# Kernel optimization log

Hardware: AMD Instinct MI355X
Metric: run time of the kernel (lower is better)

Reference implementation:

```python
import jax, jax.numpy as jnp
import numpy as np

NUM_HEADS = 8
NUM_POINTS = 4


def _bilinear(img, xs, ys):
    """Bilinear sample with zero padding (grid_sample align_corners=False).
    img: [N, H, W, C]; xs, ys: [N, P] pixel-space coords. Returns [N, P, C]."""
    H, W = img.shape[1], img.shape[2]
    x0 = jnp.floor(xs)
    y0 = jnp.floor(ys)
    wx = xs - x0
    wy = ys - y0
    x0i = x0.astype(jnp.int32)
    y0i = y0.astype(jnp.int32)

    def g(ix, iy):
        valid = ((ix >= 0) & (ix < W) & (iy >= 0) & (iy < H)).astype(img.dtype)
        ixc = jnp.clip(ix, 0, W - 1)
        iyc = jnp.clip(iy, 0, H - 1)
        v = jax.vmap(lambda im, yy, xx: im[yy, xx])(img, iyc, ixc)  # [N,P,C]
        return v * valid[..., None]

    return (g(x0i, y0i) * ((1 - wx) * (1 - wy))[..., None]
            + g(x0i + 1, y0i) * (wx * (1 - wy))[..., None]
            + g(x0i, y0i + 1) * ((1 - wx) * wy)[..., None]
            + g(x0i + 1, y0i + 1) * (wx * wy)[..., None])


def setup_inputs() -> dict:
    key = jax.random.key(0)
    ks = jax.random.split(key, 10)
    BN, C, H, W = 12, 256, 40, 100
    nq = H * W
    hp = NUM_HEADS * NUM_POINTS
    s = 1.0 / np.sqrt(C).astype(np.float32)
    return {
        "img_feats": jax.random.normal(ks[0], (BN, C, H, W), jnp.float32),
        "warp_grid": jax.random.uniform(ks[1], (BN, H, W, 2), jnp.float32),
        "reference_points": jax.random.uniform(ks[2], (BN, nq, 1, 2), jnp.float32),
        "Wv": jax.random.normal(ks[3], (C, C), jnp.float32) * s,
        "bv": jnp.zeros((C,), jnp.float32),
        "Woff": jax.random.normal(ks[4], (C, hp * 2), jnp.float32) * 0.01,
        "boff": jax.random.normal(ks[5], (hp * 2,), jnp.float32) * 0.5,
        "Wattn": jax.random.normal(ks[6], (C, hp), jnp.float32) * 0.01,
        "battn": jnp.zeros((hp,), jnp.float32),
        "Wout": jax.random.normal(ks[7], (C, C), jnp.float32) * s,
        "bout": jnp.zeros((C,), jnp.float32),
    }


def reference(img_feats, warp_grid, reference_points,
              Wv, bv, Woff, boff, Wattn, battn, Wout, bout):
    BN, C, H, W = img_feats.shape
    heads, pts = NUM_HEADS, NUM_POINTS
    hd = C // heads
    nq = H * W

    feat = img_feats.transpose(0, 2, 3, 1)  # [BN, H, W, C]

    # BEVWarp: bilinear warp of image features at the projected grid ([0,1] normed)
    gx = warp_grid[..., 0].reshape(BN, -1) * W - 0.5
    gy = warp_grid[..., 1].reshape(BN, -1) * H - 0.5
    warped = _bilinear(feat, gx, gy)          # [BN, nq, C] -> value
    query = feat.reshape(BN, nq, C)           # flattened img feats -> query

    # MultiScaleDeformableAttention, num_levels=1
    v = (warped @ Wv + bv).reshape(BN, nq, heads, hd)
    off = (query @ Woff + boff).reshape(BN, nq, heads, pts, 2)
    attn = jax.nn.softmax((query @ Wattn + battn).reshape(BN, nq, heads, pts), axis=-1)

    norm = jnp.array([W, H], dtype=img_feats.dtype)
    loc = reference_points.reshape(BN, nq, 1, 1, 2) + off / norm  # [BN,nq,h,p,2]

    vh = v.transpose(0, 2, 1, 3).reshape(BN * heads, H, W, hd)
    lx = (loc[..., 0] * W - 0.5).transpose(0, 2, 1, 3).reshape(BN * heads, nq * pts)
    ly = (loc[..., 1] * H - 0.5).transpose(0, 2, 1, 3).reshape(BN * heads, nq * pts)
    sampled = _bilinear(vh, lx, ly).reshape(BN, heads, nq, pts, hd)

    agg = jnp.einsum('bhqpd,bqhp->bqhd', sampled, attn).reshape(BN, nq, C)
    out = agg @ Wout + bout + query  # output_proj + residual (dropout=0 at eval)
    return out.transpose(0, 2, 1).reshape(BN, C, H, W)
```

## Files before the change

### kernel.cpp

```cpp
#include <hip/hip_runtime.h>

#define DEVINL __device__ __forceinline__

typedef __attribute__((ext_vector_type(4))) float f32x4;
typedef __attribute__((ext_vector_type(8))) short short8;

constexpr int kBN = 12, kC = 256, kH = 40, kW = 100;
constexpr int kNQ = kH * kW;
constexpr int kM = kBN * kNQ;

DEVINL float bflo(uint p) { union { uint i; float f; } v; v.i = p << 16; return v.f; }
DEVINL float bfhi(uint p) { union { uint i; float f; } v; v.i = p & 0xffff0000u; return v.f; }
DEVINL ushort f2bf(float f) {
  union { float f; uint i; } v; v.f = f;
  uint i = v.i;
  return (ushort)((i + 0x7fffu + ((i >> 16) & 1u)) >> 16);
}
DEVINL uint pack2(float a, float b) { return (uint)f2bf(a) | ((uint)f2bf(b) << 16); }

DEVINL void mfma_bf16(f32x4& acc, short8 a, short8 b) {
  acc = __builtin_amdgcn_mfma_f32_16x16x32_bf16(a, b, acc, 0, 0, 0);
}

DEVINL void gload16(const ushort* g, char* lds) {
  __builtin_amdgcn_global_load_lds(
      (const __attribute__((address_space(1))) uint*)g,
      (__attribute__((address_space(3))) uint*)lds, 16, 0, 0);
}

DEVINL void acc8(float* acc, uint4 d, float wv) {
  acc[0] += wv * bflo(d.x); acc[1] += wv * bfhi(d.x);
  acc[2] += wv * bflo(d.y); acc[3] += wv * bfhi(d.y);
  acc[4] += wv * bflo(d.z); acc[5] += wv * bfhi(d.z);
  acc[6] += wv * bflo(d.w); acc[7] += wv * bfhi(d.w);
}

__global__ __launch_bounds__(256) void k_wt(const float* __restrict__ W,
                                            ushort* __restrict__ WT, int K, int N) {
  int idx = blockIdx.x * 256 + threadIdx.x;
  if (idx >= K * N) return;
  int n = idx / K, k = idx - n * K;
  WT[idx] = f2bf(W[k * N + n]);
}

__global__ __launch_bounds__(256) void k_transpose(const float* __restrict__ img,
                                                   ushort* __restrict__ feat) {
  __shared__ ushort tile[64][66];
  int b = blockIdx.z, c0 = blockIdx.y * 64, q0 = blockIdx.x * 64;
  int t = threadIdx.x;
  int ql = t & 63, cl = t >> 6;
#pragma unroll
  for (int i = 0; i < 16; ++i) {
    int c = cl + i * 4, q = q0 + ql;
    float v = (q < kNQ) ? img[(size_t)(b * kC + c0 + c) * kNQ + q] : 0.f;
    tile[c][ql] = f2bf(v);
  }
  __syncthreads();
  int cc = t & 63, qr = t >> 6;
#pragma unroll
  for (int i = 0; i < 16; ++i) {
    int qlo = qr + i * 4, q = q0 + qlo;
    if (q < kNQ) feat[(size_t)(b * kNQ + q) * kC + c0 + cc] = tile[cc][qlo];
  }
}

__global__ __launch_bounds__(256) void k_warp(const ushort* __restrict__ feat,
                                              const float* __restrict__ grid,
                                              ushort* __restrict__ warped) {
  int orig = blockIdx.x;
  int n = (orig & 7) * 750 + (orig >> 3);
  int t = threadIdx.x;
  int ql = t >> 5, g = t & 31;
  int gq = n * 8 + ql;
  int b = gq / kNQ;
  float gx = grid[(size_t)gq * 2 + 0] * kW - 0.5f;
  float gy = grid[(size_t)gq * 2 + 1] * kH - 0.5f;
  float x0f = floorf(gx), y0f = floorf(gy);
  int x0 = (int)x0f, y0 = (int)y0f;
  float wx = gx - x0f, wy = gy - y0f;
  float acc[8];
#pragma unroll
  for (int i = 0; i < 8; ++i) acc[i] = 0.f;
  const ushort* fb = feat + (size_t)b * kNQ * kC + g * 8;
#pragma unroll
  for (int ty = 0; ty < 2; ++ty) {
    int iy = y0 + ty;
    if (iy < 0 || iy >= kH) continue;
    float wyv = ty ? wy : 1.f - wy;
#pragma unroll
    for (int tx = 0; tx < 2; ++tx) {
      int ix = x0 + tx;
      if (ix < 0 || ix >= kW) continue;
      float wv = wyv * (tx ? wx : 1.f - wx);
      uint4 d = *(const uint4*)(fb + (size_t)(iy * kW + ix) * kC);
      acc8(acc, d, wv);
    }
  }
  uint o[4] = {pack2(acc[0], acc[1]), pack2(acc[2], acc[3]),
               pack2(acc[4], acc[5]), pack2(acc[6], acc[7])};
  *(uint4*)(warped + (size_t)gq * kC + g * 8) = *(uint4*)o;
}

template <int EPI>
__global__ __launch_bounds__(256) void k_gemm256(const ushort* __restrict__ A,
                                                 const ushort* __restrict__ BT,
                                                 const float* __restrict__ bias,
                                                 ushort* __restrict__ Obf,
                                                 float* __restrict__ Ofp,
                                                 const float* __restrict__ resid) {
  extern __shared__ char smem[];
  char* As = smem;
  char* Bs = smem + 4096;
  const int t = threadIdx.x, wave = t >> 6, lane = t & 63;
  const int l15 = lane & 15, l4 = lane >> 4;
  const int b = blockIdx.x / 63, mb = blockIdx.x % 63;
  const int q0 = mb * 64;
  const int nrows = (kNQ - q0 < 64) ? (kNQ - q0) : 64;
  const int n0w = wave * 64;
  const int ra = t >> 2, ca = t & 3;
  const int sca = ca ^ ((ra >> 1) & 3);
  const ushort* gA = A + ((size_t)b * kNQ + q0 + ra) * 256 + sca * 8;
  const ushort* gB = BT + (size_t)ra * 256 + sca * 8;
  const bool doA = (ra < nrows);

  f32x4 acc[4][4];
#pragma unroll
  for (int i = 0; i < 4; ++i)
#pragma unroll
    for (int j = 0; j < 4; ++j) acc[i][j] = (f32x4)0.f;

  for (int kk = 0; kk < 256; kk += 32) {
    if (doA) gload16(gA + kk, As + t * 16);
#pragma unroll
    for (int i = 0; i < 4; ++i)
      gload16(gB + (size_t)i * 64 * 256 + kk, Bs + (i * 256 + t) * 16);
    __syncthreads();
    short8 af[4], bf[4];
#pragma unroll
    for (int mf = 0; mf < 4; ++mf) {
      int r = mf * 16 + l15;
      int sl = l4 ^ ((r >> 1) & 3);
      af[mf] = *(const short8*)(As + r * 64 + sl * 16);
    }
#pragma unroll
    for (int nf = 0; nf < 4; ++nf) {
      int r = n0w + nf * 16 + l15;
      int sl = l4 ^ ((r >> 1) & 3);
      bf[nf] = *(const short8*)(Bs + r * 64 + sl * 16);
    }
#pragma unroll
    for (int mf = 0; mf < 4; ++mf)
#pragma unroll
      for (int nf = 0; nf < 4; ++nf) mfma_bf16(acc[mf][nf], af[mf], bf[nf]);
    __syncthreads();
  }

  if (EPI == 0) {
#pragma unroll
    for (int mf = 0; mf < 4; ++mf) {
      if (mf * 16 >= nrows) continue;
      int q = q0 + mf * 16 + l4 * 4;
#pragma unroll
      for (int nf = 0; nf < 4; ++nf) {
        int col = n0w + nf * 16 + l15;
        float bv = bias[col];
        int h = col >> 5, ch = col & 31;
        ushort* dst = Obf + (size_t)(b * 8 + h) * kNQ * 32 + ch;
#pragma unroll
        for (int j = 0; j < 4; ++j)
          dst[(size_t)(q + j) * 32] = f2bf(acc[mf][nf][j] + bv);
      }
    }
  } else {
    float* Tw = (float*)(smem + wave * 4352);
#pragma unroll
    for (int nf = 0; nf < 4; ++nf) {
      float bv = bias[n0w + nf * 16 + l15];
#pragma unroll
      for (int mf = 0; mf < 4; ++mf)
#pragma unroll
        for (int j = 0; j < 4; ++j)
          Tw[l15 * 68 + mf * 16 + l4 * 4 + j] = acc[mf][nf][j] + bv;
      int c = l15, hi = l4;
      int rs = hi * 16;
      if (rs < nrows) {
        int col = n0w + nf * 16 + c;
        size_t gi = ((size_t)b * kC + col) * kNQ + q0 + rs;
#pragma unroll
        for (int k = 0; k < 4; ++k) {
          float4 tv = *(float4*)(&Tw[c * 68 + rs + k * 4]);
          float4 rv = *(const float4*)(resid + gi + k * 4);
          tv.x += rv.x; tv.y += rv.y; tv.z += rv.z; tv.w += rv.w;
          *(float4*)(Ofp + gi + k * 4) = tv;
        }
      }
    }
  }
}

__global__ __launch_bounds__(256) void k_offattn(const ushort* __restrict__ A,
                                                 const ushort* __restrict__ WoffT,
                                                 const ushort* __restrict__ WattnT,
                                                 const float* __restrict__ boff,
                                                 const float* __restrict__ battn,
                                                 const float* __restrict__ refp,
                                                 float4* __restrict__ samp) {
  extern __shared__ char smem[];
  char* As = smem;
  char* Bs = smem + 4096;
  float* T = (float*)smem;
  const int t = threadIdx.x, wave = t >> 6, lane = t & 63;
  const int l15 = lane & 15, l4 = lane >> 4;
  const int b = blockIdx.x / 63, mb = blockIdx.x % 63;
  const int q0 = mb * 64;
  const int nrows = (kNQ - q0 < 64) ? (kNQ - q0) : 64;
  const int wr = wave >> 1, wc = wave & 1;
  const int ra = t >> 2, ca = t & 3;
  const int sca = ca ^ ((ra >> 1) & 3);
  const ushort* gA = A + ((size_t)b * kNQ + q0 + ra) * 256 + sca * 8;
  const ushort* gB0 = WoffT + (size_t)ra * 256 + sca * 8;
  const ushort* gB1 = WattnT + (size_t)ra * 256 + sca * 8;
  const bool doA = (ra < nrows);

  f32x4 acc[2][3];
#pragma unroll
  for (int i = 0; i < 2; ++i)
#pragma unroll
    for (int j = 0; j < 3; ++j) acc[i][j] = (f32x4)0.f;

  for (int kk = 0; kk < 256; kk += 32) {
    if (doA) gload16(gA + kk, As + t * 16);
    gload16(gB0 + kk, Bs + t * 16);
    if (t < 128) gload16(gB1 + kk, Bs + (256 + t) * 16);
    __syncthreads();
    short8 af[2], bf[3];
#pragma unroll
    for (int mf = 0; mf < 2; ++mf) {
      int r = wr * 32 + mf * 16 + l15;
      int sl = l4 ^ ((r >> 1) & 3);
      af[mf] = *(const short8*)(As + r * 64 + sl * 16);
    }
#pragma unroll
    for (int nf = 0; nf < 3; ++nf) {
      int r = wc * 48 + nf * 16 + l15;
      int sl = l4 ^ ((r >> 1) & 3);
      bf[nf] = *(const short8*)(Bs + r * 64 + sl * 16);
    }
#pragma unroll
    for (int mf = 0; mf < 2; ++mf)
#pragma unroll
      for (int nf = 0; nf < 3; ++nf) mfma_bf16(acc[mf][nf], af[mf], bf[nf]);
    __syncthreads();
  }

#pragma unroll
  for (int nf = 0; nf < 3; ++nf) {
    int col = wc * 48 + nf * 16 + l15;
    float bv = (col < 64) ? boff[col] : battn[col - 64];
#pragma unroll
    for (int mf = 0; mf < 2; ++mf)
#pragma unroll
      for (int j = 0; j < 4; ++j) {
        int row = wr * 32 + mf * 16 + l4 * 4 + j;
        T[row * 101 + col] = acc[mf][nf][j] + bv;
      }
  }
  __syncthreads();
  int row = t >> 2;
  if (row < nrows) {
    int q = q0 + row;
    float refx = refp[((size_t)b * kNQ + q) * 2 + 0] * kW - 0.5f;
    float refy = refp[((size_t)b * kNQ + q) * 2 + 1] * kH - 0.5f;
#pragma unroll
    for (int hi2 = 0; hi2 < 2; ++hi2) {
      int h = (t & 3) + hi2 * 4;
      float sx[4], sy[4], lg[4];
#pragma unroll
      for (int p = 0; p < 4; ++p) {
        sx[p] = refx + T[row * 101 + h * 8 + p * 2 + 0];
        sy[p] = refy + T[row * 101 + h * 8 + p * 2 + 1];
        lg[p] = T[row * 101 + 64 + h * 4 + p];
      }
      float mx = fmaxf(fmaxf(lg[0], lg[1]), fmaxf(lg[2], lg[3]));
      float e[4], s = 0.f;
#pragma unroll
      for (int p = 0; p < 4; ++p) { e[p] = __expf(lg[p] - mx); s += e[p]; }
      float inv = 1.f / s;
      float4* dst = samp + ((size_t)(b * 8 + h) * kNQ + q) * 4;
#pragma unroll
      for (int p = 0; p < 4; ++p) dst[p] = make_float4(sx[p], sy[p], e[p] * inv, 0.f);
    }
  }
}

__global__ __launch_bounds__(256) void k_sample(const ushort* __restrict__ v,
                                                const float4* __restrict__ samp,
                                                ushort* __restrict__ agg) {
  int orig = blockIdx.x;
  int n = (orig & 7) * 756 + (orig >> 3);
  int plane = n / 63, chunk = n - plane * 63;
  int t = threadIdx.x;
  int ql = t >> 2, g = t & 3;
  int q = chunk * 64 + ql;
  if (q >= kNQ) return;
  int b = plane >> 3, h = plane & 7;
  const ushort* pv = v + (size_t)plane * kNQ * 32 + g * 8;
  const int lane = t & 63, gbase = lane & ~3;

  float4 mys = samp[((size_t)plane * kNQ + q) * 4 + g];
  float acc[8];
#pragma unroll
  for (int i = 0; i < 8; ++i) acc[i] = 0.f;
#pragma unroll
  for (int p = 0; p < 4; ++p) {
    float sxp = __shfl(mys.x, gbase + p);
    float syp = __shfl(mys.y, gbase + p);
    float wp  = __shfl(mys.z, gbase + p);
    float x0f = floorf(sxp), y0f = floorf(syp);
    int x0 = (int)x0f, y0 = (int)y0f;
    float wx = sxp - x0f, wy = syp - y0f;
#pragma unroll
    for (int ty = 0; ty < 2; ++ty) {
      int iy = y0 + ty;
      if (iy < 0 || iy >= kH) continue;
      float wyv = ty ? wy : 1.f - wy;
#pragma unroll
      for (int tx = 0; tx < 2; ++tx) {
        int ix = x0 + tx;
        if (ix < 0 || ix >= kW) continue;
        float wv = wp * wyv * (tx ? wx : 1.f - wx);
        uint4 d = *(const uint4*)(pv + (size_t)(iy * kW + ix) * 32);
        acc8(acc, d, wv);
      }
    }
  }
  uint o[4] = {pack2(acc[0], acc[1]), pack2(acc[2], acc[3]),
               pack2(acc[4], acc[5]), pack2(acc[6], acc[7])};
  *(uint4*)(agg + ((size_t)b * kNQ + q) * kC + h * 32 + g * 8) = *(uint4*)o;
}

extern "C" void kernel_launch(void* const* d_in, const int* in_sizes, int n_in,
                              void* d_out, int out_size, void* d_ws, size_t ws_size,
                              hipStream_t stream) {
  const float* img   = (const float*)d_in[0];
  const float* grid  = (const float*)d_in[1];
  const float* refp  = (const float*)d_in[2];
  const float* Wv    = (const float*)d_in[3];
  const float* bv    = (const float*)d_in[4];
  const float* Woff  = (const float*)d_in[5];
  const float* boff  = (const float*)d_in[6];
  const float* Wattn = (const float*)d_in[7];
  const float* battn = (const float*)d_in[8];
  const float* Wout  = (const float*)d_in[9];
  const float* bout  = (const float*)d_in[10];
  float* out = (float*)d_out;

  char* ws = (char*)d_ws;
  const size_t SZ = (size_t)kM * kC * 2;
  ushort* feat   = (ushort*)(ws);
  ushort* warped = (ushort*)(ws + SZ);
  ushort* vbuf   = (ushort*)(ws + 2 * SZ);
  float4* samp   = (float4*)(ws + 3 * SZ);
  ushort* WvT    = (ushort*)(ws + 4 * SZ);
  ushort* WoffT  = (ushort*)(ws + 4 * SZ + 131072);
  ushort* WattnT = (ushort*)(ws + 4 * SZ + 131072 + 32768);
  ushort* WoutT  = (ushort*)(ws + 4 * SZ + 131072 + 32768 + 16384);
  ushort* aggb   = warped;

  k_wt<<<(65536 + 255) / 256, 256, 0, stream>>>(Wv, WvT, 256, 256);
  k_wt<<<(16384 + 255) / 256, 256, 0, stream>>>(Woff, WoffT, 256, 64);
  k_wt<<<(8192 + 255) / 256, 256, 0, stream>>>(Wattn, WattnT, 256, 32);
  k_wt<<<(65536 + 255) / 256, 256, 0, stream>>>(Wout, WoutT, 256, 256);

  k_transpose<<<dim3(63, 4, 12), 256, 0, stream>>>(img, feat);
  k_warp<<<6000, 256, 0, stream>>>(feat, grid, warped);
  k_gemm256<0><<<756, 256, 20480, stream>>>(warped, WvT, bv, vbuf, nullptr, nullptr);
  k_offattn<<<756, 256, 25856, stream>>>(feat, WoffT, WattnT, boff, battn, refp, samp);
  k_sample<<<6048, 256, 0, stream>>>(vbuf, samp, aggb);
  k_gemm256<1><<<756, 256, 20480, stream>>>(aggb, WoutT, bout, nullptr, out, img);
}
```

Measured before the change: 135.1 us.

## Fuse offset/attn GEMM, deformable sampling and output projection into one kernel

Merges the offset/attention projection, softmax, bilinear deformable sampling and output projection with residual into a single per-tile kernel. The sample parameters and aggregated values now stay in LDS instead of round-tripping through global memory. The four weight-transpose launches are also merged into one, and block indices are remapped across XCDs. In exchange the fused kernel needs about 58KB of LDS, which lowers occupancy, and the gather phase uses only 756 blocks with a serial loop over heads, so latency hiding during sampling may drop.

After: 162.1 us. 1.2x slower.

```diff
diff --git a/kernel.cpp b/kernel.cpp
--- a/kernel.cpp
+++ b/kernel.cpp
@@ -35,12 +35,24 @@
   acc[6] += wv * bflo(d.w); acc[7] += wv * bfhi(d.w);
 }
 
-__global__ __launch_bounds__(256) void k_wt(const float* __restrict__ W,
-                                            ushort* __restrict__ WT, int K, int N) {
+__global__ __launch_bounds__(256) void k_wt_all(const float* __restrict__ Wv,
+                                                const float* __restrict__ Woff,
+                                                const float* __restrict__ Wattn,
+                                                const float* __restrict__ Wout,
+                                                ushort* __restrict__ WvT,
+                                                ushort* __restrict__ WoffT,
+                                                ushort* __restrict__ WattnT,
+                                                ushort* __restrict__ WoutT) {
   int idx = blockIdx.x * 256 + threadIdx.x;
-  if (idx >= K * N) return;
-  int n = idx / K, k = idx - n * K;
-  WT[idx] = f2bf(W[k * N + n]);
+  const float* W; ushort* WT; int N, base;
+  if (idx < 65536)       { W = Wv;    WT = WvT;    N = 256; base = 0; }
+  else if (idx < 81920)  { W = Woff;  WT = WoffT;  N = 64;  base = 65536; }
+  else if (idx < 90112)  { W = Wattn; WT = WattnT; N = 32;  base = 81920; }
+  else if (idx < 155648) { W = Wout;  WT = WoutT;  N = 256; base = 90112; }
+  else return;
+  int i = idx - base;
+  int n = i >> 8, k = i & 255;
+  WT[i] = f2bf(W[k * N + n]);
 }
 
 __global__ __launch_bounds__(256) void k_transpose(const float* __restrict__ img,
@@ -101,13 +113,10 @@
   *(uint4*)(warped + (size_t)gq * kC + g * 8) = *(uint4*)o;
 }
 
-template <int EPI>
-__global__ __launch_bounds__(256) void k_gemm256(const ushort* __restrict__ A,
-                                                 const ushort* __restrict__ BT,
-                                                 const float* __restrict__ bias,
-                                                 ushort* __restrict__ Obf,
-                                                 float* __restrict__ Ofp,
-                                                 const float* __restrict__ resid) {
+__global__ __launch_bounds__(256) void k_gemmv(const ushort* __restrict__ A,
+                                               const ushort* __restrict__ BT,
+                                               const float* __restrict__ bias,
+                                               ushort* __restrict__ Obf) {
   extern __shared__ char smem[];
   char* As = smem;
   char* Bs = smem + 4096;
@@ -155,118 +164,107 @@
     __syncthreads();
   }
 
-  if (EPI == 0) {
-#pragma unroll
-    for (int mf = 0; mf < 4; ++mf) {
-      if (mf * 16 >= nrows) continue;
-      int q = q0 + mf * 16 + l4 * 4;
-#pragma unroll
-      for (int nf = 0; nf < 4; ++nf) {
-        int col = n0w + nf * 16 + l15;
-        float bv = bias[col];
-        int h = col >> 5, ch = col & 31;
-        ushort* dst = Obf + (size_t)(b * 8 + h) * kNQ * 32 + ch;
-#pragma unroll
-        for (int j = 0; j < 4; ++j)
-          dst[(size_t)(q + j) * 32] = f2bf(acc[mf][nf][j] + bv);
-      }
-    }
-  } else {
-    float* Tw = (float*)(smem + wave * 4352);
+#pragma unroll
+  for (int mf = 0; mf < 4; ++mf) {
+    if (mf * 16 >= nrows) continue;
+    int q = q0 + mf * 16 + l4 * 4;
 #pragma unroll
     for (int nf = 0; nf < 4; ++nf) {
-      float bv = bias[n0w + nf * 16 + l15];
-#pragma unroll
-      for (int mf = 0; mf < 4; ++mf)
-#pragma unroll
-        for (int j = 0; j < 4; ++j)
-          Tw[l15 * 68 + mf * 16 + l4 * 4 + j] = acc[mf][nf][j] + bv;
-      int c = l15, hi = l4;
-      int rs = hi * 16;
-      if (rs < nrows) {
-        int col = n0w + nf * 16 + c;
-        size_t gi = ((size_t)b * kC + col) * kNQ + q0 + rs;
-#pragma unroll
-        for (int k = 0; k < 4; ++k) {
-          float4 tv = *(float4*)(&Tw[c * 68 + rs + k * 4]);
-          float4 rv = *(const float4*)(resid + gi + k * 4);
-          tv.x += rv.x; tv.y += rv.y; tv.z += rv.z; tv.w += rv.w;
-          *(float4*)(Ofp + gi + k * 4) = tv;
-        }
-      }
-    }
-  }
-}
-
-__global__ __launch_bounds__(256) void k_offattn(const ushort* __restrict__ A,
-                                                 const ushort* __restrict__ WoffT,
-                                                 const ushort* __restrict__ WattnT,
-                                                 const float* __restrict__ boff,
-                                                 const float* __restrict__ battn,
-                                                 const float* __restrict__ refp,
-                                                 float4* __restrict__ samp) {
+      int col = n0w + nf * 16 + l15;
+      float bv = bias[col];
+      int h = col >> 5, ch = col & 31;
+      ushort* dst = Obf + (size_t)(b * 8 + h) * kNQ * 32 + ch;
+#pragma unroll
+      for (int j = 0; j < 4; ++j)
+        dst[(size_t)(q + j) * 32] = f2bf(acc[mf][nf][j] + bv);
+    }
+  }
+}
+
+__global__ __launch_bounds__(256) void k_mega(const ushort* __restrict__ feat,
+                                              const ushort* __restrict__ WoffT,
+                                              const ushort* __restrict__ WattnT,
+                                              const float* __restrict__ boff,
+                                              const float* __restrict__ battn,
+                                              const float* __restrict__ refp,
+                                              const ushort* __restrict__ vbuf,
+                                              const ushort* __restrict__ WoutT,
+                                              const float* __restrict__ bout,
+                                              const float* __restrict__ resid,
+                                              float* __restrict__ out) {
   extern __shared__ char smem[];
-  char* As = smem;
-  char* Bs = smem + 4096;
-  float* T = (float*)smem;
+  float* T  = (float*)smem;
+  char* As1 = smem + 26624;
+  char* Bs1 = smem + 26624 + 4096;
+  char* Ag  = smem + 26624;
+  char* Bs3 = smem;
+
   const int t = threadIdx.x, wave = t >> 6, lane = t & 63;
   const int l15 = lane & 15, l4 = lane >> 4;
-  const int b = blockIdx.x / 63, mb = blockIdx.x % 63;
+
+  int orig = blockIdx.x;
+  int xcd = orig % 8, ii = orig / 8;
+  int n = (xcd < 4 ? xcd * 95 : 380 + (xcd - 4) * 94) + ii;
+  const int b = n / 63, mb = n % 63;
   const int q0 = mb * 64;
   const int nrows = (kNQ - q0 < 64) ? (kNQ - q0) : 64;
+
   const int wr = wave >> 1, wc = wave & 1;
   const int ra = t >> 2, ca = t & 3;
   const int sca = ca ^ ((ra >> 1) & 3);
-  const ushort* gA = A + ((size_t)b * kNQ + q0 + ra) * 256 + sca * 8;
+  const ushort* gA  = feat + ((size_t)b * kNQ + q0 + ra) * 256 + sca * 8;
   const ushort* gB0 = WoffT + (size_t)ra * 256 + sca * 8;
   const ushort* gB1 = WattnT + (size_t)ra * 256 + sca * 8;
   const bool doA = (ra < nrows);
 
-  f32x4 acc[2][3];
-#pragma unroll
-  for (int i = 0; i < 2; ++i)
-#pragma unroll
-    for (int j = 0; j < 3; ++j) acc[i][j] = (f32x4)0.f;
-
-  for (int kk = 0; kk < 256; kk += 32) {
-    if (doA) gload16(gA + kk, As + t * 16);
-    gload16(gB0 + kk, Bs + t * 16);
-    if (t < 128) gload16(gB1 + kk, Bs + (256 + t) * 16);
-    __syncthreads();
-    short8 af[2], bf[3];
-#pragma unroll
-    for (int mf = 0; mf < 2; ++mf) {
-      int r = wr * 32 + mf * 16 + l15;
-      int sl = l4 ^ ((r >> 1) & 3);
-      af[mf] = *(const short8*)(As + r * 64 + sl * 16);
-    }
+  {
+    f32x4 acc1[2][3];
+#pragma unroll
+    for (int i = 0; i < 2; ++i)
+#pragma unroll
+      for (int j = 0; j < 3; ++j) acc1[i][j] = (f32x4)0.f;
+
+    for (int kk = 0; kk < 256; kk += 32) {
+      if (doA) gload16(gA + kk, As1 + t * 16);
+      gload16(gB0 + kk, Bs1 + t * 16);
+      if (t < 128) gload16(gB1 + kk, Bs1 + (256 + t) * 16);
+      __syncthreads();
+      short8 af[2], bf[3];
+#pragma unroll
+      for (int mf = 0; mf < 2; ++mf) {
+        int r = wr * 32 + mf * 16 + l15;
+        int sl = l4 ^ ((r >> 1) & 3);
+        af[mf] = *(const short8*)(As1 + r * 64 + sl * 16);
+      }
+#pragma unroll
+      for (int nf = 0; nf < 3; ++nf) {
+        int r = wc * 48 + nf * 16 + l15;
+        int sl = l4 ^ ((r >> 1) & 3);
+        bf[nf] = *(const short8*)(Bs1 + r * 64 + sl * 16);
+      }
+#pragma unroll
+      for (int mf = 0; mf < 2; ++mf)
+#pragma unroll
+        for (int nf = 0; nf < 3; ++nf) mfma_bf16(acc1[mf][nf], af[mf], bf[nf]);
+      __syncthreads();
+    }
+
 #pragma unroll
     for (int nf = 0; nf < 3; ++nf) {
-      int r = wc * 48 + nf * 16 + l15;
-      int sl = l4 ^ ((r >> 1) & 3);
-      bf[nf] = *(const short8*)(Bs + r * 64 + sl * 16);
-    }
-#pragma unroll
-    for (int mf = 0; mf < 2; ++mf)
-#pragma unroll
-      for (int nf = 0; nf < 3; ++nf) mfma_bf16(acc[mf][nf], af[mf], bf[nf]);
-    __syncthreads();
-  }
-
-#pragma unroll
-  for (int nf = 0; nf < 3; ++nf) {
-    int col = wc * 48 + nf * 16 + l15;
-    float bv = (col < 64) ? boff[col] : battn[col - 64];
-#pragma unroll
-    for (int mf = 0; mf < 2; ++mf)
-#pragma unroll
-      for (int j = 0; j < 4; ++j) {
-        int row = wr * 32 + mf * 16 + l4 * 4 + j;
-        T[row * 101 + col] = acc[mf][nf][j] + bv;
-      }
+      int col = wc * 48 + nf * 16 + l15;
+      float bv = (col < 64) ? boff[col] : battn[col - 64];
+#pragma unroll
+      for (int mf = 0; mf < 2; ++mf)
+#pragma unroll
+        for (int j = 0; j < 4; ++j) {
+          int row = wr * 32 + mf * 16 + l4 * 4 + j;
+          T[row * 101 + col] = acc1[mf][nf][j] + bv;
+        }
+    }
   }
   __syncthreads();
-  int row = t >> 2;
+
+  const int row = t >> 2;
   if (row < nrows) {
     int q = q0 + row;
     float refx = refp[((size_t)b * kNQ + q) * 2 + 0] * kW - 0.5f;
@@ -286,57 +284,108 @@
 #pragma unroll
       for (int p = 0; p < 4; ++p) { e[p] = __expf(lg[p] - mx); s += e[p]; }
       float inv = 1.f / s;
-      float4* dst = samp + ((size_t)(b * 8 + h) * kNQ + q) * 4;
-#pragma unroll
-      for (int p = 0; p < 4; ++p) dst[p] = make_float4(sx[p], sy[p], e[p] * inv, 0.f);
-    }
-  }
-}
-
-__global__ __launch_bounds__(256) void k_sample(const ushort* __restrict__ v,
-                                                const float4* __restrict__ samp,
-                                                ushort* __restrict__ agg) {
-  int orig = blockIdx.x;
-  int n = (orig & 7) * 756 + (orig >> 3);
-  int plane = n / 63, chunk = n - plane * 63;
-  int t = threadIdx.x;
-  int ql = t >> 2, g = t & 3;
-  int q = chunk * 64 + ql;
-  if (q >= kNQ) return;
-  int b = plane >> 3, h = plane & 7;
-  const ushort* pv = v + (size_t)plane * kNQ * 32 + g * 8;
-  const int lane = t & 63, gbase = lane & ~3;
-
-  float4 mys = samp[((size_t)plane * kNQ + q) * 4 + g];
-  float acc[8];
-#pragma unroll
-  for (int i = 0; i < 8; ++i) acc[i] = 0.f;
-#pragma unroll
-  for (int p = 0; p < 4; ++p) {
-    float sxp = __shfl(mys.x, gbase + p);
-    float syp = __shfl(mys.y, gbase + p);
-    float wp  = __shfl(mys.z, gbase + p);
-    float x0f = floorf(sxp), y0f = floorf(syp);
-    int x0 = (int)x0f, y0 = (int)y0f;
-    float wx = sxp - x0f, wy = syp - y0f;
-#pragma unroll
-    for (int ty = 0; ty < 2; ++ty) {
-      int iy = y0 + ty;
-      if (iy < 0 || iy >= kH) continue;
-      float wyv = ty ? wy : 1.f - wy;
-#pragma unroll
-      for (int tx = 0; tx < 2; ++tx) {
-        int ix = x0 + tx;
-        if (ix < 0 || ix >= kW) continue;
-        float wv = wp * wyv * (tx ? wx : 1.f - wx);
-        uint4 d = *(const uint4*)(pv + (size_t)(iy * kW + ix) * 32);
-        acc8(acc, d, wv);
-      }
-    }
-  }
-  uint o[4] = {pack2(acc[0], acc[1]), pack2(acc[2], acc[3]),
-               pack2(acc[4], acc[5]), pack2(acc[6], acc[7])};
-  *(uint4*)(agg + ((size_t)b * kNQ + q) * kC + h * 32 + g * 8) = *(uint4*)o;
+#pragma unroll
+      for (int p = 0; p < 4; ++p) {
+        T[row * 101 + h * 8 + p * 2 + 0] = sx[p];
+        T[row * 101 + h * 8 + p * 2 + 1] = sy[p];
+        T[row * 101 + 64 + h * 4 + p] = e[p] * inv;
+      }
+    }
+  }
+  __syncthreads();
+
+  if (row < nrows) {
+    int g = t & 3;
+    for (int h = 0; h < 8; ++h) {
+      const ushort* pv = vbuf + (size_t)(b * 8 + h) * kNQ * 32 + g * 8;
+      float acc[8];
+#pragma unroll
+      for (int i = 0; i < 8; ++i) acc[i] = 0.f;
+#pragma unroll
+      for (int p = 0; p < 4; ++p) {
+        float sxp = T[row * 101 + h * 8 + p * 2 + 0];
+        float syp = T[row * 101 + h * 8 + p * 2 + 1];
+        float wp  = T[row * 101 + 64 + h * 4 + p];
+        float x0f = floorf(sxp), y0f = floorf(syp);
+        int x0 = (int)x0f, y0 = (int)y0f;
+        float wx = sxp - x0f, wy = syp - y0f;
+#pragma unroll
+        for (int ty = 0; ty < 2; ++ty) {
+          int iy = y0 + ty;
+          if (iy < 0 || iy >= kH) continue;
+          float wyv = ty ? wy : 1.f - wy;
+#pragma unroll
+          for (int tx = 0; tx < 2; ++tx) {
+            int ix = x0 + tx;
+            if (ix < 0 || ix >= kW) continue;
+            float wv = wp * wyv * (tx ? wx : 1.f - wx);
+            uint4 d = *(const uint4*)(pv + (size_t)(iy * kW + ix) * 32);
+            acc8(acc, d, wv);
+          }
+        }
+      }
+      uint o[4] = {pack2(acc[0], acc[1]), pack2(acc[2], acc[3]),
+                   pack2(acc[4], acc[5]), pack2(acc[6], acc[7])};
+      int byteoff = (row * 512 + h * 64 + g * 16) ^ ((row & 7) << 4);
+      *(uint4*)(Ag + byteoff) = *(uint4*)o;
+    }
+  }
+  __syncthreads();
+
+  const int n0w = wave * 64;
+  f32x4 acc3[4][4];
+#pragma unroll
+  for (int i = 0; i < 4; ++i)
+#pragma unroll
+    for (int j = 0; j < 4; ++j) acc3[i][j] = (f32x4)0.f;
+  const ushort* gB3 = WoutT + (size_t)ra * 256 + sca * 8;
+
+  for (int kk = 0; kk < 256; kk += 32) {
+#pragma unroll
+    for (int i = 0; i < 4; ++i)
+      gload16(gB3 + (size_t)i * 64 * 256 + kk, Bs3 + (i * 256 + t) * 16);
+    __syncthreads();
+    short8 af[4], bf[4];
+#pragma unroll
+    for (int mf = 0; mf < 4; ++mf) {
+      int r = mf * 16 + l15;
+      af[mf] = *(const short8*)(Ag + ((r * 512 + kk * 2 + l4 * 16) ^ ((r & 7) << 4)));
+    }
+#pragma unroll
+    for (int nf = 0; nf < 4; ++nf) {
+      int r = n0w + nf * 16 + l15;
+      int sl = l4 ^ ((r >> 1) & 3);
+      bf[nf] = *(const short8*)(Bs3 + r * 64 + sl * 16);
+    }
+#pragma unroll
+    for (int mf = 0; mf < 4; ++mf)
+#pragma unroll
+      for (int nf = 0; nf < 4; ++nf) mfma_bf16(acc3[mf][nf], af[mf], bf[nf]);
+    __syncthreads();
+  }
+
+  float* Tw = (float*)(smem + wave * 4352);
+#pragma unroll
+  for (int nf = 0; nf < 4; ++nf) {
+    float bv = bout[n0w + nf * 16 + l15];
+#pragma unroll
+    for (int mf = 0; mf < 4; ++mf)
+#pragma unroll
+      for (int j = 0; j < 4; ++j)
+        Tw[l15 * 68 + mf * 16 + l4 * 4 + j] = acc3[mf][nf][j] + bv;
+    int c = l15, rs = l4 * 16;
+    if (rs < nrows) {
+      int col = n0w + nf * 16 + c;
+      size_t gi = ((size_t)b * kC + col) * kNQ + q0 + rs;
+#pragma unroll
+      for (int k = 0; k < 4; ++k) {
+        float4 tv = *(float4*)(&Tw[c * 68 + rs + k * 4]);
+        float4 rv = *(const float4*)(resid + gi + k * 4);
+        tv.x += rv.x; tv.y += rv.y; tv.z += rv.z; tv.w += rv.w;
+        *(float4*)(out + gi + k * 4) = tv;
+      }
+    }
+  }
 }
 
 extern "C" void kernel_launch(void* const* d_in, const int* in_sizes, int n_in,
@@ -360,22 +409,15 @@
   ushort* feat   = (ushort*)(ws);
   ushort* warped = (ushort*)(ws + SZ);
   ushort* vbuf   = (ushort*)(ws + 2 * SZ);
-  float4* samp   = (float4*)(ws + 3 * SZ);
-  ushort* WvT    = (ushort*)(ws + 4 * SZ);
-  ushort* WoffT  = (ushort*)(ws + 4 * SZ + 131072);
-  ushort* WattnT = (ushort*)(ws + 4 * SZ + 131072 + 32768);
-  ushort* WoutT  = (ushort*)(ws + 4 * SZ + 131072 + 32768 + 16384);
-  ushort* aggb   = warped;
-
-  k_wt<<<(65536 + 255) / 256, 256, 0, stream>>>(Wv, WvT, 256, 256);
-  k_wt<<<(16384 + 255) / 256, 256, 0, stream>>>(Woff, WoffT, 256, 64);
-  k_wt<<<(8192 + 255) / 256, 256, 0, stream>>>(Wattn, WattnT, 256, 32);
-  k_wt<<<(65536 + 255) / 256, 256, 0, stream>>>(Wout, WoutT, 256, 256);
-
+  ushort* WvT    = (ushort*)(ws + 3 * SZ);
+  ushort* WoffT  = (ushort*)(ws + 3 * SZ + 131072);
+  ushort* WattnT = (ushort*)(ws + 3 * SZ + 131072 + 32768);
+  ushort* WoutT  = (ushort*)(ws + 3 * SZ + 131072 + 32768 + 16384);
+
+  k_wt_all<<<608, 256, 0, stream>>>(Wv, Woff, Wattn, Wout, WvT, WoffT, WattnT, WoutT);
   k_transpose<<<dim3(63, 4, 12), 256, 0, stream>>>(img, feat);
   k_warp<<<6000, 256, 0, stream>>>(feat, grid, warped);
-  k_gemm256<0><<<756, 256, 20480, stream>>>(warped, WvT, bv, vbuf, nullptr, nullptr);
-  k_offattn<<<756, 256, 25856, stream>>>(feat, WoffT, WattnT, boff, battn, refp, samp);
-  k_sample<<<6048, 256, 0, stream>>>(vbuf, samp, aggb);
-  k_gemm256<1><<<756, 256, 20480, stream>>>(aggb, WoutT, bout, nullptr, out, img);
-}
+  k_gemmv<<<756, 256, 20480, stream>>>(warped, WvT, bv, vbuf);
+  k_mega<<<756, 256, 59392, stream>>>(feat, WoffT, WattnT, boff, battn, refp,
+                                      vbuf, WoutT, bout, img, out);
+}
```

## Double-buffer LDS tiles in GEMM kernels and merge weight transpose launches

Applied to the files above, without the earlier changes.

The k-loops of the 256-wide GEMM and the offset/attention GEMM now use two LDS buffers. The next k-slice's global-to-LDS loads are issued before computing on the current one, so one barrier per step remains and load latency can overlap the MFMAs. The four weight-transpose kernel launches are folded into a single launch. The larger LDS footprint for the main GEMM could reduce blocks resident per CU.

After: 128.5 us. 1.05x faster.

```diff
diff --git a/kernel.cpp b/kernel.cpp
--- a/kernel.cpp
+++ b/kernel.cpp
@@ -35,12 +35,24 @@
   acc[6] += wv * bflo(d.w); acc[7] += wv * bfhi(d.w);
 }
 
-__global__ __launch_bounds__(256) void k_wt(const float* __restrict__ W,
-                                            ushort* __restrict__ WT, int K, int N) {
+__global__ __launch_bounds__(256) void k_wt_all(const float* __restrict__ Wv,
+                                                const float* __restrict__ Woff,
+                                                const float* __restrict__ Wattn,
+                                                const float* __restrict__ Wout,
+                                                ushort* __restrict__ WvT,
+                                                ushort* __restrict__ WoffT,
+                                                ushort* __restrict__ WattnT,
+                                                ushort* __restrict__ WoutT) {
   int idx = blockIdx.x * 256 + threadIdx.x;
-  if (idx >= K * N) return;
-  int n = idx / K, k = idx - n * K;
-  WT[idx] = f2bf(W[k * N + n]);
+  const float* W; ushort* WT; int N, base;
+  if (idx < 65536)       { W = Wv;    WT = WvT;    N = 256; base = 0; }
+  else if (idx < 81920)  { W = Woff;  WT = WoffT;  N = 64;  base = 65536; }
+  else if (idx < 90112)  { W = Wattn; WT = WattnT; N = 32;  base = 81920; }
+  else if (idx < 155648) { W = Wout;  WT = WoutT;  N = 256; base = 90112; }
+  else return;
+  int i = idx - base;
+  int n = i >> 8, k = i & 255;
+  WT[i] = f2bf(W[k * N + n]);
 }
 
 __global__ __launch_bounds__(256) void k_transpose(const float* __restrict__ img,
@@ -109,8 +121,6 @@
                                                  float* __restrict__ Ofp,
                                                  const float* __restrict__ resid) {
   extern __shared__ char smem[];
-  char* As = smem;
-  char* Bs = smem + 4096;
   const int t = threadIdx.x, wave = t >> 6, lane = t & 63;
   const int l15 = lane & 15, l4 = lane >> 4;
   const int b = blockIdx.x / 63, mb = blockIdx.x % 63;
@@ -129,30 +139,42 @@
 #pragma unroll
     for (int j = 0; j < 4; ++j) acc[i][j] = (f32x4)0.f;
 
-  for (int kk = 0; kk < 256; kk += 32) {
-    if (doA) gload16(gA + kk, As + t * 16);
+  auto STAGE = [&](int buf, int kk) {
+    char* Asb = smem + buf * 20480;
+    char* Bsb = Asb + 4096;
+    if (doA) gload16(gA + kk, Asb + t * 16);
 #pragma unroll
     for (int i = 0; i < 4; ++i)
-      gload16(gB + (size_t)i * 64 * 256 + kk, Bs + (i * 256 + t) * 16);
-    __syncthreads();
+      gload16(gB + (size_t)i * 64 * 256 + kk, Bsb + (i * 256 + t) * 16);
+  };
+
+  STAGE(0, 0);
+  __syncthreads();
+  int cur = 0;
+#pragma unroll 1
+  for (int step = 0; step < 8; ++step) {
+    if (step < 7) STAGE(cur ^ 1, (step + 1) * 32);
+    char* Asb = smem + cur * 20480;
+    char* Bsb = Asb + 4096;
     short8 af[4], bf[4];
 #pragma unroll
     for (int mf = 0; mf < 4; ++mf) {
       int r = mf * 16 + l15;
       int sl = l4 ^ ((r >> 1) & 3);
-      af[mf] = *(const short8*)(As + r * 64 + sl * 16);
+      af[mf] = *(const short8*)(Asb + r * 64 + sl * 16);
     }
 #pragma unroll
     for (int nf = 0; nf < 4; ++nf) {
       int r = n0w + nf * 16 + l15;
       int sl = l4 ^ ((r >> 1) & 3);
-      bf[nf] = *(const short8*)(Bs + r * 64 + sl * 16);
+      bf[nf] = *(const short8*)(Bsb + r * 64 + sl * 16);
     }
 #pragma unroll
     for (int mf = 0; mf < 4; ++mf)
 #pragma unroll
       for (int nf = 0; nf < 4; ++nf) mfma_bf16(acc[mf][nf], af[mf], bf[nf]);
     __syncthreads();
+    cur ^= 1;
   }
 
   if (EPI == 0) {
@@ -181,8 +203,7 @@
 #pragma unroll
         for (int j = 0; j < 4; ++j)
           Tw[l15 * 68 + mf * 16 + l4 * 4 + j] = acc[mf][nf][j] + bv;
-      int c = l15, hi = l4;
-      int rs = hi * 16;
+      int c = l15, rs = l4 * 16;
       if (rs < nrows) {
         int col = n0w + nf * 16 + c;
         size_t gi = ((size_t)b * kC + col) * kNQ + q0 + rs;
@@ -206,8 +227,6 @@
                                                  const float* __restrict__ refp,
                                                  float4* __restrict__ samp) {
   extern __shared__ char smem[];
-  char* As = smem;
-  char* Bs = smem + 4096;
   float* T = (float*)smem;
   const int t = threadIdx.x, wave = t >> 6, lane = t & 63;
   const int l15 = lane & 15, l4 = lane >> 4;
@@ -217,7 +236,7 @@
   const int wr = wave >> 1, wc = wave & 1;
   const int ra = t >> 2, ca = t & 3;
   const int sca = ca ^ ((ra >> 1) & 3);
-  const ushort* gA = A + ((size_t)b * kNQ + q0 + ra) * 256 + sca * 8;
+  const ushort* gA  = A + ((size_t)b * kNQ + q0 + ra) * 256 + sca * 8;
   const ushort* gB0 = WoffT + (size_t)ra * 256 + sca * 8;
   const ushort* gB1 = WattnT + (size_t)ra * 256 + sca * 8;
   const bool doA = (ra < nrows);
@@ -228,29 +247,41 @@
 #pragma unroll
     for (int j = 0; j < 3; ++j) acc[i][j] = (f32x4)0.f;
 
-  for (int kk = 0; kk < 256; kk += 32) {
-    if (doA) gload16(gA + kk, As + t * 16);
-    gload16(gB0 + kk, Bs + t * 16);
-    if (t < 128) gload16(gB1 + kk, Bs + (256 + t) * 16);
-    __syncthreads();
+  auto STAGE = [&](int buf, int kk) {
+    char* Asb = smem + buf * 10240;
+    char* Bsb = Asb + 4096;
+    if (doA) gload16(gA + kk, Asb + t * 16);
+    gload16(gB0 + kk, Bsb + t * 16);
+    if (t < 128) gload16(gB1 + kk, Bsb + (256 + t) * 16);
+  };
+
+  STAGE(0, 0);
+  __syncthreads();
+  int cur = 0;
+#pragma unroll 1
+  for (int step = 0; step < 8; ++step) {
+    if (step < 7) STAGE(cur ^ 1, (step + 1) * 32);
+    char* Asb = smem + cur * 10240;
+    char* Bsb = Asb + 4096;
     short8 af[2], bf[3];
 #pragma unroll
     for (int mf = 0; mf < 2; ++mf) {
       int r = wr * 32 + mf * 16 + l15;
       int sl = l4 ^ ((r >> 1) & 3);
-      af[mf] = *(const short8*)(As + r * 64 + sl * 16);
+      af[mf] = *(const short8*)(Asb + r * 64 + sl * 16);
     }
 #pragma unroll
     for (int nf = 0; nf < 3; ++nf) {
       int r = wc * 48 + nf * 16 + l15;
       int sl = l4 ^ ((r >> 1) & 3);
-      bf[nf] = *(const short8*)(Bs + r * 64 + sl * 16);
+      bf[nf] = *(const short8*)(Bsb + r * 64 + sl * 16);
     }
 #pragma unroll
     for (int mf = 0; mf < 2; ++mf)
 #pragma unroll
       for (int nf = 0; nf < 3; ++nf) mfma_bf16(acc[mf][nf], af[mf], bf[nf]);
     __syncthreads();
+    cur ^= 1;
   }
 
 #pragma unroll
@@ -367,15 +398,11 @@
   ushort* WoutT  = (ushort*)(ws + 4 * SZ + 131072 + 32768 + 16384);
   ushort* aggb   = warped;
 
-  k_wt<<<(65536 + 255) / 256, 256, 0, stream>>>(Wv, WvT, 256, 256);
-  k_wt<<<(16384 + 255) / 256, 256, 0, stream>>>(Woff, WoffT, 256, 64);
-  k_wt<<<(8192 + 255) / 256, 256, 0, stream>>>(Wattn, WattnT, 256, 32);
-  k_wt<<<(65536 + 255) / 256, 256, 0, stream>>>(Wout, WoutT, 256, 256);
-
+  k_wt_all<<<608, 256, 0, stream>>>(Wv, Woff, Wattn, Wout, WvT, WoffT, WattnT, WoutT);
   k_transpose<<<dim3(63, 4, 12), 256, 0, stream>>>(img, feat);
   k_warp<<<6000, 256, 0, stream>>>(feat, grid, warped);
-  k_gemm256<0><<<756, 256, 20480, stream>>>(warped, WvT, bv, vbuf, nullptr, nullptr);
+  k_gemm256<0><<<756, 256, 40960, stream>>>(warped, WvT, bv, vbuf, nullptr, nullptr);
   k_offattn<<<756, 256, 25856, stream>>>(feat, WoffT, WattnT, boff, battn, refp, samp);
   k_sample<<<6048, 256, 0, stream>>>(vbuf, samp, aggb);
-  k_gemm256<1><<<756, 256, 20480, stream>>>(aggb, WoutT, bout, nullptr, out, img);
-}
+  k_gemm256<1><<<756, 256, 40960, stream>>>(aggb, WoutT, bout, nullptr, out, img);
+}
```
